# Kernel tuning notes

Measured on AMD Instinct MI355X. Metric: run time of the kernel, lower is better.

## Reference

```python
import jax, jax.numpy as jnp
import numpy as np

T = 32
BATCH = 1024
LATENT = 1024
HIDDEN = 1024


def setup_inputs() -> dict:
    key = jax.random.key(0)
    ks = jax.random.split(key, 13)
    s = 0.02
    return {
        "latent": jax.random.normal(ks[0], (BATCH, LATENT), jnp.float32),
        "h0": jax.random.normal(ks[1], (BATCH, HIDDEN), jnp.float32),
        "c0": jax.random.normal(ks[2], (BATCH, HIDDEN), jnp.float32),
        # LSTM kernel (input dim = 2*LATENT), recurrent kernel, bias; gate order i,f,g,o
        "Wk": jax.random.normal(ks[3], (2 * LATENT, 4 * HIDDEN), jnp.float32) * s,
        "Wr": jax.random.normal(ks[4], (HIDDEN, 4 * HIDDEN), jnp.float32) * s,
        "b": jnp.zeros((4 * HIDDEN,), jnp.float32),
        # attention: w1 on latent, w2 on concat(h,c)
        "W1": jax.random.normal(ks[5], (LATENT, LATENT), jnp.float32) * s,
        "b1": jnp.zeros((LATENT,), jnp.float32),
        "W2": jax.random.normal(ks[6], (2 * HIDDEN, LATENT), jnp.float32) * s,
        "b2": jnp.zeros((LATENT,), jnp.float32),
        # output mu dense
        "Wmu": jax.random.normal(ks[7], (HIDDEN, 1), jnp.float32) * s,
        "bmu": jnp.zeros((1,), jnp.float32),
    }


def _attention_context(h, c, latent, W1, b1, W2, b2):
    # score: (batch, latent_dims); softmax over feature axis (axis=1) as in the original
    query = jnp.concatenate([h, c], axis=-1)
    score = jnp.tanh(latent @ W1 + b1 + query @ W2 + b2)
    beta = jax.nn.softmax(score, axis=1)
    return beta * latent


def reference(latent, h0, c0, Wk, Wr, b, W1, b1, W2, b2, Wmu, bmu):
    # initial attention/context from h0, c0
    context = _attention_context(h0, c0, latent, W1, b1, W2, b2)

    def step(carry, _):
        h, c, ctx = carry
        x = jnp.concatenate([latent, ctx], axis=-1)  # (batch, 2*latent)
        z = x @ Wk + h @ Wr + b                       # (batch, 4*hidden)
        i, f, g, o = jnp.split(z, 4, axis=-1)         # keras gate order i,f,c,o
        c_new = jax.nn.sigmoid(f) * c + jax.nn.sigmoid(i) * jnp.tanh(g)
        h_new = jax.nn.sigmoid(o) * jnp.tanh(c_new)
        ctx_new = _attention_context(h_new, c_new, latent, W1, b1, W2, b2)
        out = h_new @ Wmu + bmu                        # (batch, 1)
        return (h_new, c_new, ctx_new), out

    _, outs = jax.lax.scan(step, (h0, c0, context), None, length=T)
    # outs: (T, batch, 1) -> (batch, T, 1)
    return jnp.transpose(outs, (1, 0, 2))
```

## Files before the change

kernel.cpp:

```cpp
#include <hip/hip_runtime.h>


#define T_ 32

typedef __attribute__((ext_vector_type(8))) short short8;
typedef __attribute__((ext_vector_type(4))) float f32x4;

__device__ __forceinline__ unsigned short bf16u(float x) {
  unsigned int u = __float_as_uint(x);
  u += 0x7FFFu + ((u >> 16) & 1u);
  return (unsigned short)(u >> 16);
}
__device__ __forceinline__ float b2f(unsigned short u) {
  return __uint_as_float(((unsigned int)u) << 16);
}
__device__ __forceinline__ ushort4 pack4(float a, float b, float c, float d) {
  ushort4 v; v.x = bf16u(a); v.y = bf16u(b); v.z = bf16u(c); v.w = bf16u(d); return v;
}
__device__ __forceinline__ float sigmoidf_(float x) { return 1.f / (1.f + __expf(-x)); }
__device__ __forceinline__ float tanhf_(float x) { return 1.f - 2.f / (__expf(2.f * x) + 1.f); }

__global__ void k_transpose(const float* __restrict__ src, int srcN,
                            unsigned short* __restrict__ dst, int dstStride, int dstColOff) {
  __shared__ float tile[32][33];
  int n0 = blockIdx.x * 32, k0 = blockIdx.y * 32;
  int tx = threadIdx.x, ty = threadIdx.y;
#pragma unroll
  for (int i = 0; i < 4; ++i)
    tile[ty + i * 8][tx] = src[(size_t)(k0 + ty + i * 8) * srcN + n0 + tx];
  __syncthreads();
#pragma unroll
  for (int i = 0; i < 4; ++i)
    dst[(size_t)(n0 + ty + i * 8) * dstStride + dstColOff + k0 + tx] = bf16u(tile[tx][ty + i * 8]);
}

__global__ __launch_bounds__(256) void k_init(const float* __restrict__ h0,
                                              const float* __restrict__ c0,
                                              const float* __restrict__ latent,
                                              unsigned short* __restrict__ A1,
                                              unsigned short* __restrict__ A2,
                                              unsigned short* __restrict__ latbf,
                                              float* __restrict__ c_st) {
  int r = blockIdx.x; int j = threadIdx.x * 4;
  const float4 hv = *(const float4*)&h0[(size_t)r * 1024 + j];
  const float4 cv = *(const float4*)&c0[(size_t)r * 1024 + j];
  const float4 lv = *(const float4*)&latent[(size_t)r * 1024 + j];
  *(ushort4*)&A2[(size_t)r * 2048 + j]        = pack4(hv.x, hv.y, hv.z, hv.w);
  *(ushort4*)&A2[(size_t)r * 2048 + 1024 + j] = pack4(cv.x, cv.y, cv.z, cv.w);
  *(ushort4*)&A1[(size_t)r * 2048 + 1024 + j] = pack4(hv.x, hv.y, hv.z, hv.w);
  *(ushort4*)&latbf[(size_t)r * 1024 + j]     = pack4(lv.x, lv.y, lv.z, lv.w);
  *(float4*)&c_st[(size_t)r * 1024 + j] = cv;
}

__global__ void k_bias(const float* __restrict__ b1, const float* __restrict__ b2,
                       float* __restrict__ bias_s) {
  int i = blockIdx.x * 256 + threadIdx.x;
  bias_s[i] = b1[i] + b2[i];
}

__global__ __launch_bounds__(256) void k_gemm(const unsigned short* __restrict__ A, int lda,
                                              const unsigned short* __restrict__ Bt, int ldb,
                                              int Kchunk,
                                              const float* __restrict__ bias,
                                              float* __restrict__ Cf,
                                              unsigned short* __restrict__ Cb, int N) {
  __shared__ unsigned short Al[2][128 * 64];
  __shared__ unsigned short Bl[2][128 * 64];
  const int tid = threadIdx.x;
  const int w = tid >> 6, l = tid & 63;
  const int row0 = blockIdx.y * 128, col0 = blockIdx.x * 128;
  const int wr = (w >> 1) * 64, wc = (w & 1) * 64;
  const int lr = l & 15, lkb = (l >> 4) * 8;
  const int srow = (l >> 3);
  const int scol_src = ((l & 7) ^ srow) * 8;
  const int kbeg = blockIdx.z * Kchunk;
  const int nsteps = Kchunk >> 6;

  f32x4 acc[4][4] = {};

  auto stage = [&](int buf, int k0) {
#pragma unroll
    for (int it = 0; it < 4; ++it) {
      int chunk = w * 4 + it;
      int r = chunk * 8 + srow;
      const unsigned short* ga = A + (size_t)(row0 + r) * lda + k0 + scol_src;
      const unsigned short* gb = Bt + (size_t)(col0 + r) * ldb + k0 + scol_src;
      __builtin_amdgcn_global_load_lds(
          (const __attribute__((address_space(1))) unsigned int*)ga,
          (__attribute__((address_space(3))) unsigned int*)((char*)&Al[buf][0] + chunk * 1024), 16, 0, 0);
      __builtin_amdgcn_global_load_lds(
          (const __attribute__((address_space(1))) unsigned int*)gb,
          (__attribute__((address_space(3))) unsigned int*)((char*)&Bl[buf][0] + chunk * 1024), 16, 0, 0);
    }
  };

  stage(0, kbeg);
  __syncthreads();
  int cur = 0;
  for (int s = 0; s < nsteps; ++s) {
    if (s + 1 < nsteps) stage(cur ^ 1, kbeg + (s + 1) * 64);
#pragma unroll
    for (int kk = 0; kk < 2; ++kk) {
      const int c2 = kk * 64 + (l >> 4) * 16;
      short8 a[4], b[4];
#pragma unroll
      for (int m = 0; m < 4; ++m) {
        int r = wr + m * 16 + lr;
        a[m] = *(const short8*)((char*)&Al[cur][0] + r * 128 + (c2 ^ ((r & 7) << 4)));
      }
#pragma unroll
      for (int n = 0; n < 4; ++n) {
        int r = wc + n * 16 + lr;
        b[n] = *(const short8*)((char*)&Bl[cur][0] + r * 128 + (c2 ^ ((r & 7) << 4)));
      }
#pragma unroll
      for (int m = 0; m < 4; ++m)
#pragma unroll
        for (int n = 0; n < 4; ++n)
          acc[m][n] = __builtin_amdgcn_mfma_f32_16x16x32_bf16(a[m], b[n], acc[m][n], 0, 0, 0);
    }
    __syncthreads();
    cur ^= 1;
  }

  const int rbase = (l >> 4) * 4;
  if (Cf) {
#pragma unroll
    for (int m = 0; m < 4; ++m)
#pragma unroll
      for (int rg = 0; rg < 4; ++rg) {
        int row = row0 + wr + m * 16 + rbase + rg;
#pragma unroll
        for (int n = 0; n < 4; ++n) {
          int col = col0 + wc + n * 16 + lr;
          Cf[(size_t)row * N + col] = acc[m][n][rg] + bias[col];
        }
      }
  } else {
    unsigned short* Cp = Cb + (size_t)blockIdx.z * (size_t)(gridDim.y * 128) * N;
#pragma unroll
    for (int m = 0; m < 4; ++m)
#pragma unroll
      for (int rg = 0; rg < 4; ++rg) {
        int row = row0 + wr + m * 16 + rbase + rg;
#pragma unroll
        for (int n = 0; n < 4; ++n) {
          int col = col0 + wc + n * 16 + lr;
          Cp[(size_t)row * N + col] = bf16u(acc[m][n][rg]);
        }
      }
  }
}

__global__ __launch_bounds__(256) void k_lstm(const float* __restrict__ z_lat,
                                              const unsigned short* __restrict__ zp,
                                              float* __restrict__ c_st,
                                              unsigned short* __restrict__ A1,
                                              unsigned short* __restrict__ A2,
                                              const float* __restrict__ Wmu,
                                              const float* __restrict__ bmu,
                                              float* __restrict__ out, int t) {
  __shared__ float red[4];
  const size_t Z1 = (size_t)1024 * 4096;
  int r = blockIdx.x; int tid = threadIdx.x; int j = tid * 4;
  float g4[4][4];
#pragma unroll
  for (int g = 0; g < 4; ++g) {
    const float4 zl = *(const float4*)&z_lat[(size_t)r * 4096 + g * 1024 + j];
    const ushort4 p0 = *(const ushort4*)&zp[(size_t)r * 4096 + g * 1024 + j];
    const ushort4 p1 = *(const ushort4*)&zp[Z1 + (size_t)r * 4096 + g * 1024 + j];
    g4[g][0] = zl.x + b2f(p0.x) + b2f(p1.x);
    g4[g][1] = zl.y + b2f(p0.y) + b2f(p1.y);
    g4[g][2] = zl.z + b2f(p0.z) + b2f(p1.z);
    g4[g][3] = zl.w + b2f(p0.w) + b2f(p1.w);
  }
  const float4 cv = *(const float4*)&c_st[(size_t)r * 1024 + j];
  const float4 wm = *(const float4*)&Wmu[j];
  float cc[4] = {cv.x, cv.y, cv.z, cv.w}, wv[4] = {wm.x, wm.y, wm.z, wm.w};
  float cn[4], hn[4];
  float part = 0.f;
#pragma unroll
  for (int q = 0; q < 4; ++q) {
    float c2 = sigmoidf_(g4[1][q]) * cc[q] + sigmoidf_(g4[0][q]) * tanhf_(g4[2][q]);
    float h2 = sigmoidf_(g4[3][q]) * tanhf_(c2);
    cn[q] = c2; hn[q] = h2; part += h2 * wv[q];
  }
  *(float4*)&c_st[(size_t)r * 1024 + j] = make_float4(cn[0], cn[1], cn[2], cn[3]);
  *(ushort4*)&A2[(size_t)r * 2048 + j]        = pack4(hn[0], hn[1], hn[2], hn[3]);
  *(ushort4*)&A2[(size_t)r * 2048 + 1024 + j] = pack4(cn[0], cn[1], cn[2], cn[3]);
  *(ushort4*)&A1[(size_t)r * 2048 + 1024 + j] = pack4(hn[0], hn[1], hn[2], hn[3]);
#pragma unroll
  for (int off = 32; off > 0; off >>= 1) part += __shfl_down(part, off, 64);
  if ((tid & 63) == 0) red[tid >> 6] = part;
  __syncthreads();
  if (tid == 0) out[(size_t)r * T_ + t] = red[0] + red[1] + red[2] + red[3] + bmu[0];
}

__global__ __launch_bounds__(256) void k_attn(const float* __restrict__ s_lat,
                                              const unsigned short* __restrict__ sp8,
                                              const float* __restrict__ latent,
                                              unsigned short* __restrict__ A1) {
  __shared__ float red[4];
  const size_t P = (size_t)1024 * 1024;
  int r = blockIdx.x; int tid = threadIdx.x; int j = tid * 4;
  const float4 sl = *(const float4*)&s_lat[(size_t)r * 1024 + j];
  float sv[4] = {sl.x, sl.y, sl.z, sl.w};
#pragma unroll
  for (int sidx = 0; sidx < 8; ++sidx) {
    const ushort4 q = *(const ushort4*)&sp8[sidx * P + (size_t)r * 1024 + j];
    sv[0] += b2f(q.x); sv[1] += b2f(q.y); sv[2] += b2f(q.z); sv[3] += b2f(q.w);
  }
  float s[4] = {tanhf_(sv[0]), tanhf_(sv[1]), tanhf_(sv[2]), tanhf_(sv[3])};
  float mx = fmaxf(fmaxf(s[0], s[1]), fmaxf(s[2], s[3]));
#pragma unroll
  for (int off = 32; off > 0; off >>= 1) mx = fmaxf(mx, __shfl_xor(mx, off, 64));
  if ((tid & 63) == 0) red[tid >> 6] = mx;
  __syncthreads();
  mx = fmaxf(fmaxf(red[0], red[1]), fmaxf(red[2], red[3]));
  __syncthreads();
  float e[4], ps = 0.f;
#pragma unroll
  for (int q = 0; q < 4; ++q) { e[q] = __expf(s[q] - mx); ps += e[q]; }
#pragma unroll
  for (int off = 32; off > 0; off >>= 1) ps += __shfl_xor(ps, off, 64);
  if ((tid & 63) == 0) red[tid >> 6] = ps;
  __syncthreads();
  float inv = 1.f / (red[0] + red[1] + red[2] + red[3]);
  const float4 lv = *(const float4*)&latent[(size_t)r * 1024 + j];
  float lvv[4] = {lv.x, lv.y, lv.z, lv.w};
  *(ushort4*)&A1[(size_t)r * 2048 + j] =
      pack4(e[0] * inv * lvv[0], e[1] * inv * lvv[1], e[2] * inv * lvv[2], e[3] * inv * lvv[3]);
}

extern "C" void kernel_launch(void* const* d_in, const int* in_sizes, int n_in,
                              void* d_out, int out_size, void* d_ws, size_t ws_size,
                              hipStream_t stream) {
  const float* latent = (const float*)d_in[0];
  const float* h0  = (const float*)d_in[1];
  const float* c0  = (const float*)d_in[2];
  const float* Wk  = (const float*)d_in[3];
  const float* Wr  = (const float*)d_in[4];
  const float* b   = (const float*)d_in[5];
  const float* W1  = (const float*)d_in[6];
  const float* b1  = (const float*)d_in[7];
  const float* W2  = (const float*)d_in[8];
  const float* b2  = (const float*)d_in[9];
  const float* Wmu = (const float*)d_in[10];
  const float* bmu = (const float*)d_in[11];
  float* out = (float*)d_out;

  char* p = (char*)d_ws;
  auto alloc = [&](size_t bytes) { void* r = (void*)p; p += (bytes + 255) & ~(size_t)255; return r; };
  unsigned short* Wzh_t = (unsigned short*)alloc((size_t)4096 * 2048 * 2);
  unsigned short* Wk1_t = (unsigned short*)alloc((size_t)4096 * 1024 * 2);
  unsigned short* W1t   = (unsigned short*)alloc((size_t)1024 * 1024 * 2);
  unsigned short* W2t   = (unsigned short*)alloc((size_t)1024 * 2048 * 2);
  unsigned short* latbf = (unsigned short*)alloc((size_t)1024 * 1024 * 2);
  unsigned short* A1    = (unsigned short*)alloc((size_t)1024 * 2048 * 2);
  unsigned short* A2    = (unsigned short*)alloc((size_t)1024 * 2048 * 2);
  float* z_lat  = (float*)alloc((size_t)1024 * 4096 * 4);
  float* s_lat  = (float*)alloc((size_t)1024 * 1024 * 4);
  unsigned short* z_part = (unsigned short*)alloc((size_t)2 * 1024 * 4096 * 2);
  unsigned short* spre_p = (unsigned short*)alloc((size_t)8 * 1024 * 1024 * 2);
  float* c_st   = (float*)alloc((size_t)1024 * 1024 * 4);
  float* bias_s = (float*)alloc((size_t)1024 * 4);

  dim3 tb(32, 8);
  k_transpose<<<dim3(128, 32), tb, 0, stream>>>(Wk, 4096, Wk1_t, 1024, 0);
  k_transpose<<<dim3(128, 32), tb, 0, stream>>>(Wk + (size_t)1024 * 4096, 4096, Wzh_t, 2048, 0);
  k_transpose<<<dim3(128, 32), tb, 0, stream>>>(Wr, 4096, Wzh_t, 2048, 1024);
  k_transpose<<<dim3(32, 64), tb, 0, stream>>>(W2, 1024, W2t, 2048, 0);
  k_transpose<<<dim3(32, 32), tb, 0, stream>>>(W1, 1024, W1t, 1024, 0);

  k_init<<<1024, 256, 0, stream>>>(h0, c0, latent, A1, A2, latbf, c_st);
  k_bias<<<4, 256, 0, stream>>>(b1, b2, bias_s);

  k_gemm<<<dim3(32, 8, 1), 256, 0, stream>>>(latbf, 1024, Wk1_t, 1024, 1024, b, z_lat, nullptr, 4096);
  k_gemm<<<dim3(8, 8, 1), 256, 0, stream>>>(latbf, 1024, W1t, 1024, 1024, bias_s, s_lat, nullptr, 1024);

  k_gemm<<<dim3(8, 8, 8), 256, 0, stream>>>(A2, 2048, W2t, 2048, 256, nullptr, nullptr, spre_p, 1024);
  k_attn<<<1024, 256, 0, stream>>>(s_lat, spre_p, latent, A1);

  for (int t = 0; t < T_; ++t) {
    k_gemm<<<dim3(32, 8, 2), 256, 0, stream>>>(A1, 2048, Wzh_t, 2048, 1024, nullptr, nullptr, z_part, 4096);
    k_lstm<<<1024, 256, 0, stream>>>(z_lat, z_part, c_st, A1, A2, Wmu, bmu, out, t);
    if (t < T_ - 1) {
      k_gemm<<<dim3(8, 8, 8), 256, 0, stream>>>(A2, 2048, W2t, 2048, 256, nullptr, nullptr, spre_p, 1024);
      k_attn<<<1024, 256, 0, stream>>>(s_lat, spre_p, latent, A1);
    }
  }
}
```

Before: 1.641 ms.

## Merge attention-query and recurrent GEMMs into one launch, shrink K tile

The recurrent h@Wr product is split out of the big per-step gate GEMM and computed together with the attention query GEMM (concat(h,c)@W2) in a single combined kernel launch, since both depend only on the new h,c. The gate GEMM then only multiplies ctx@Wk_bottom and accumulates onto the precomputed bf16 partials. The K tile drops from 64 to 32 with smaller LDS buffers, and split-K for the attention GEMM goes from 8 to 4. This packs more blocks into each launch and cuts the serial K length of the critical-path GEMM. The cost is an extra bf16 read-modify-write of the partial sums, with added rounding error.

```diff
diff --git a/kernel.cpp b/kernel.cpp
--- a/kernel.cpp
+++ b/kernel.cpp
@@ -5,6 +5,7 @@
 
 typedef __attribute__((ext_vector_type(8))) short short8;
 typedef __attribute__((ext_vector_type(4))) float f32x4;
+typedef unsigned short ushort_t;
 
 __device__ __forceinline__ unsigned short bf16u(float x) {
   unsigned int u = __float_as_uint(x);
@@ -21,7 +22,7 @@
 __device__ __forceinline__ float tanhf_(float x) { return 1.f - 2.f / (__expf(2.f * x) + 1.f); }
 
 __global__ void k_transpose(const float* __restrict__ src, int srcN,
-                            unsigned short* __restrict__ dst, int dstStride, int dstColOff) {
+                            unsigned short* __restrict__ dst, int dstStride) {
   __shared__ float tile[32][33];
   int n0 = blockIdx.x * 32, k0 = blockIdx.y * 32;
   int tx = threadIdx.x, ty = threadIdx.y;
@@ -31,13 +32,12 @@
   __syncthreads();
 #pragma unroll
   for (int i = 0; i < 4; ++i)
-    dst[(size_t)(n0 + ty + i * 8) * dstStride + dstColOff + k0 + tx] = bf16u(tile[tx][ty + i * 8]);
+    dst[(size_t)(n0 + ty + i * 8) * dstStride + k0 + tx] = bf16u(tile[tx][ty + i * 8]);
 }
 
 __global__ __launch_bounds__(256) void k_init(const float* __restrict__ h0,
                                               const float* __restrict__ c0,
                                               const float* __restrict__ latent,
-                                              unsigned short* __restrict__ A1,
                                               unsigned short* __restrict__ A2,
                                               unsigned short* __restrict__ latbf,
                                               float* __restrict__ c_st) {
@@ -47,7 +47,6 @@
   const float4 lv = *(const float4*)&latent[(size_t)r * 1024 + j];
   *(ushort4*)&A2[(size_t)r * 2048 + j]        = pack4(hv.x, hv.y, hv.z, hv.w);
   *(ushort4*)&A2[(size_t)r * 2048 + 1024 + j] = pack4(cv.x, cv.y, cv.z, cv.w);
-  *(ushort4*)&A1[(size_t)r * 2048 + 1024 + j] = pack4(hv.x, hv.y, hv.z, hv.w);
   *(ushort4*)&latbf[(size_t)r * 1024 + j]     = pack4(lv.x, lv.y, lv.z, lv.w);
   *(float4*)&c_st[(size_t)r * 1024 + j] = cv;
 }
@@ -56,6 +55,60 @@
                        float* __restrict__ bias_s) {
   int i = blockIdx.x * 256 + threadIdx.x;
   bias_s[i] = b1[i] + b2[i];
+}
+
+#define GLD(src, dst)                                                                   \
+  __builtin_amdgcn_global_load_lds(                                                     \
+      (const __attribute__((address_space(1))) unsigned int*)(src),                     \
+      (__attribute__((address_space(3))) unsigned int*)(dst), 16, 0, 0)
+
+__device__ __forceinline__ void gemm_core(const unsigned short* __restrict__ A, int lda,
+                                          const unsigned short* __restrict__ Bt, int ldb,
+                                          int row0, int col0, int kbeg, int nsteps,
+                                          unsigned short* Al, unsigned short* Bl,
+                                          f32x4 acc[4][4], int w, int l) {
+  const int lr = l & 15;
+  const int slot = l >> 4;
+  const int st_row = l >> 2;
+  const int st_cole = (((l & 3) ^ ((l >> 2) & 3)) << 3);
+  const int wr = (w >> 1) * 64, wc = (w & 1) * 64;
+
+  auto stage = [&](int buf, int k0) {
+#pragma unroll
+    for (int it = 0; it < 2; ++it) {
+      int chunk = w * 2 + it;
+      int r = chunk * 16 + st_row;
+      const unsigned short* ga = A + (size_t)(row0 + r) * lda + k0 + st_cole;
+      const unsigned short* gb = Bt + (size_t)(col0 + r) * ldb + k0 + st_cole;
+      GLD(ga, (char*)Al + buf * 8192 + chunk * 1024);
+      GLD(gb, (char*)Bl + buf * 8192 + chunk * 1024);
+    }
+  };
+
+  stage(0, kbeg);
+  __syncthreads();
+  int cur = 0;
+  for (int s = 0; s < nsteps; ++s) {
+    if (s + 1 < nsteps) stage(cur ^ 1, kbeg + (s + 1) * 32);
+    short8 a[4], b[4];
+#pragma unroll
+    for (int m = 0; m < 4; ++m) {
+      int r = wr + m * 16 + lr;
+      a[m] = *(const short8*)((char*)Al + cur * 8192 + r * 64 + ((slot ^ (r & 3)) << 4));
+    }
+#pragma unroll
+    for (int n = 0; n < 4; ++n) {
+      int r = wc + n * 16 + lr;
+      b[n] = *(const short8*)((char*)Bl + cur * 8192 + r * 64 + ((slot ^ (r & 3)) << 4));
+    }
+#pragma unroll
+    for (int m = 0; m < 4; ++m)
+#pragma unroll
+      for (int n = 0; n < 4; ++n)
+        acc[m][n] = __builtin_amdgcn_mfma_f32_16x16x32_bf16(a[m], b[n], acc[m][n], 0, 0, 0);
+    __syncthreads();
+    cur ^= 1;
+  }
 }
 
 __global__ __launch_bounds__(256) void k_gemm(const unsigned short* __restrict__ A, int lda,
@@ -63,99 +116,88 @@
                                               int Kchunk,
                                               const float* __restrict__ bias,
                                               float* __restrict__ Cf,
-                                              unsigned short* __restrict__ Cb, int N) {
-  __shared__ unsigned short Al[2][128 * 64];
-  __shared__ unsigned short Bl[2][128 * 64];
-  const int tid = threadIdx.x;
-  const int w = tid >> 6, l = tid & 63;
+                                              unsigned short* __restrict__ Cb,
+                                              const unsigned short* __restrict__ addb, int N) {
+  __shared__ unsigned short Al[2][128 * 32];
+  __shared__ unsigned short Bl[2][128 * 32];
+  const int tid = threadIdx.x, w = tid >> 6, l = tid & 63;
   const int row0 = blockIdx.y * 128, col0 = blockIdx.x * 128;
-  const int wr = (w >> 1) * 64, wc = (w & 1) * 64;
-  const int lr = l & 15, lkb = (l >> 4) * 8;
-  const int srow = (l >> 3);
-  const int scol_src = ((l & 7) ^ srow) * 8;
-  const int kbeg = blockIdx.z * Kchunk;
-  const int nsteps = Kchunk >> 6;
-
   f32x4 acc[4][4] = {};
-
-  auto stage = [&](int buf, int k0) {
-#pragma unroll
-    for (int it = 0; it < 4; ++it) {
-      int chunk = w * 4 + it;
-      int r = chunk * 8 + srow;
-      const unsigned short* ga = A + (size_t)(row0 + r) * lda + k0 + scol_src;
-      const unsigned short* gb = Bt + (size_t)(col0 + r) * ldb + k0 + scol_src;
-      __builtin_amdgcn_global_load_lds(
-          (const __attribute__((address_space(1))) unsigned int*)ga,
-          (__attribute__((address_space(3))) unsigned int*)((char*)&Al[buf][0] + chunk * 1024), 16, 0, 0);
-      __builtin_amdgcn_global_load_lds(
-          (const __attribute__((address_space(1))) unsigned int*)gb,
-          (__attribute__((address_space(3))) unsigned int*)((char*)&Bl[buf][0] + chunk * 1024), 16, 0, 0);
-    }
-  };
-
-  stage(0, kbeg);
-  __syncthreads();
-  int cur = 0;
-  for (int s = 0; s < nsteps; ++s) {
-    if (s + 1 < nsteps) stage(cur ^ 1, kbeg + (s + 1) * 64);
-#pragma unroll
-    for (int kk = 0; kk < 2; ++kk) {
-      const int c2 = kk * 64 + (l >> 4) * 16;
-      short8 a[4], b[4];
-#pragma unroll
-      for (int m = 0; m < 4; ++m) {
-        int r = wr + m * 16 + lr;
-        a[m] = *(const short8*)((char*)&Al[cur][0] + r * 128 + (c2 ^ ((r & 7) << 4)));
-      }
-#pragma unroll
-      for (int n = 0; n < 4; ++n) {
-        int r = wc + n * 16 + lr;
-        b[n] = *(const short8*)((char*)&Bl[cur][0] + r * 128 + (c2 ^ ((r & 7) << 4)));
-      }
-#pragma unroll
-      for (int m = 0; m < 4; ++m)
-#pragma unroll
-        for (int n = 0; n < 4; ++n)
-          acc[m][n] = __builtin_amdgcn_mfma_f32_16x16x32_bf16(a[m], b[n], acc[m][n], 0, 0, 0);
-    }
-    __syncthreads();
-    cur ^= 1;
-  }
-
-  const int rbase = (l >> 4) * 4;
+  gemm_core(A, lda, Bt, ldb, row0, col0, blockIdx.z * Kchunk, Kchunk >> 5,
+            &Al[0][0], &Bl[0][0], acc, w, l);
+
+  const int lr = l & 15, rbase = (l >> 4) * 4;
   if (Cf) {
 #pragma unroll
     for (int m = 0; m < 4; ++m)
 #pragma unroll
       for (int rg = 0; rg < 4; ++rg) {
-        int row = row0 + wr + m * 16 + rbase + rg;
+        int row = row0 + (w >> 1) * 64 + m * 16 + rbase + rg;
 #pragma unroll
         for (int n = 0; n < 4; ++n) {
-          int col = col0 + wc + n * 16 + lr;
+          int col = col0 + (w & 1) * 64 + n * 16 + lr;
           Cf[(size_t)row * N + col] = acc[m][n][rg] + bias[col];
         }
       }
   } else {
-    unsigned short* Cp = Cb + (size_t)blockIdx.z * (size_t)(gridDim.y * 128) * N;
+    size_t zoff = (size_t)blockIdx.z * 1024 * N;
 #pragma unroll
     for (int m = 0; m < 4; ++m)
 #pragma unroll
       for (int rg = 0; rg < 4; ++rg) {
-        int row = row0 + wr + m * 16 + rbase + rg;
+        int row = row0 + (w >> 1) * 64 + m * 16 + rbase + rg;
 #pragma unroll
         for (int n = 0; n < 4; ++n) {
-          int col = col0 + wc + n * 16 + lr;
-          Cp[(size_t)row * N + col] = bf16u(acc[m][n][rg]);
+          int col = col0 + (w & 1) * 64 + n * 16 + lr;
+          size_t idx = zoff + (size_t)row * N + col;
+          float v = acc[m][n][rg];
+          if (addb) v += b2f(addb[idx]);
+          Cb[idx] = bf16u(v);
         }
       }
   }
 }
 
+__global__ __launch_bounds__(256) void k_gemm_ab(const unsigned short* __restrict__ A2,
+                                                 const unsigned short* __restrict__ W2t,
+                                                 const unsigned short* __restrict__ Wrt,
+                                                 unsigned short* __restrict__ spre_p,
+                                                 unsigned short* __restrict__ zh_p) {
+  __shared__ unsigned short Al[2][128 * 32];
+  __shared__ unsigned short Bl[2][128 * 32];
+  const int tid = threadIdx.x, w = tid >> 6, l = tid & 63;
+  int bid = blockIdx.x;
+  const unsigned short *A, *Bt; unsigned short* outp;
+  int lda, ldb, N, row0, col0, z;
+  if (bid < 256) {
+    A = A2; lda = 2048; Bt = W2t; ldb = 2048; N = 1024; outp = spre_p;
+    col0 = (bid & 7) * 128; row0 = ((bid >> 3) & 7) * 128; z = bid >> 6;
+  } else {
+    bid -= 256;
+    A = A2; lda = 2048; Bt = Wrt; ldb = 1024; N = 4096; outp = zh_p;
+    col0 = (bid & 31) * 128; row0 = ((bid >> 5) & 7) * 128; z = bid >> 8;
+  }
+  f32x4 acc[4][4] = {};
+  gemm_core(A, lda, Bt, ldb, row0, col0, z * 512, 16, &Al[0][0], &Bl[0][0], acc, w, l);
+
+  const int lr = l & 15, rbase = (l >> 4) * 4;
+  size_t zoff = (size_t)z * 1024 * N;
+#pragma unroll
+  for (int m = 0; m < 4; ++m)
+#pragma unroll
+    for (int rg = 0; rg < 4; ++rg) {
+      int row = row0 + (w >> 1) * 64 + m * 16 + rbase + rg;
+#pragma unroll
+      for (int n = 0; n < 4; ++n) {
+        int col = col0 + (w & 1) * 64 + n * 16 + lr;
+        outp[zoff + (size_t)row * N + col] = bf16u(acc[m][n][rg]);
+      }
+    }
+}
+
 __global__ __launch_bounds__(256) void k_lstm(const float* __restrict__ z_lat,
-                                              const unsigned short* __restrict__ zp,
+                                              const unsigned short* __restrict__ zsum,
                                               float* __restrict__ c_st,
-                                              unsigned short* __restrict__ A1,
                                               unsigned short* __restrict__ A2,
                                               const float* __restrict__ Wmu,
                                               const float* __restrict__ bmu,
@@ -167,8 +209,8 @@
 #pragma unroll
   for (int g = 0; g < 4; ++g) {
     const float4 zl = *(const float4*)&z_lat[(size_t)r * 4096 + g * 1024 + j];
-    const ushort4 p0 = *(const ushort4*)&zp[(size_t)r * 4096 + g * 1024 + j];
-    const ushort4 p1 = *(const ushort4*)&zp[Z1 + (size_t)r * 4096 + g * 1024 + j];
+    const ushort4 p0 = *(const ushort4*)&zsum[(size_t)r * 4096 + g * 1024 + j];
+    const ushort4 p1 = *(const ushort4*)&zsum[Z1 + (size_t)r * 4096 + g * 1024 + j];
     g4[g][0] = zl.x + b2f(p0.x) + b2f(p1.x);
     g4[g][1] = zl.y + b2f(p0.y) + b2f(p1.y);
     g4[g][2] = zl.z + b2f(p0.z) + b2f(p1.z);
@@ -188,7 +230,6 @@
   *(float4*)&c_st[(size_t)r * 1024 + j] = make_float4(cn[0], cn[1], cn[2], cn[3]);
   *(ushort4*)&A2[(size_t)r * 2048 + j]        = pack4(hn[0], hn[1], hn[2], hn[3]);
   *(ushort4*)&A2[(size_t)r * 2048 + 1024 + j] = pack4(cn[0], cn[1], cn[2], cn[3]);
-  *(ushort4*)&A1[(size_t)r * 2048 + 1024 + j] = pack4(hn[0], hn[1], hn[2], hn[3]);
 #pragma unroll
   for (int off = 32; off > 0; off >>= 1) part += __shfl_down(part, off, 64);
   if ((tid & 63) == 0) red[tid >> 6] = part;
@@ -197,17 +238,17 @@
 }
 
 __global__ __launch_bounds__(256) void k_attn(const float* __restrict__ s_lat,
-                                              const unsigned short* __restrict__ sp8,
+                                              const unsigned short* __restrict__ sp4,
                                               const float* __restrict__ latent,
-                                              unsigned short* __restrict__ A1) {
+                                              unsigned short* __restrict__ ctxb) {
   __shared__ float red[4];
   const size_t P = (size_t)1024 * 1024;
   int r = blockIdx.x; int tid = threadIdx.x; int j = tid * 4;
   const float4 sl = *(const float4*)&s_lat[(size_t)r * 1024 + j];
   float sv[4] = {sl.x, sl.y, sl.z, sl.w};
 #pragma unroll
-  for (int sidx = 0; sidx < 8; ++sidx) {
-    const ushort4 q = *(const ushort4*)&sp8[sidx * P + (size_t)r * 1024 + j];
+  for (int sidx = 0; sidx < 4; ++sidx) {
+    const ushort4 q = *(const ushort4*)&sp4[sidx * P + (size_t)r * 1024 + j];
     sv[0] += b2f(q.x); sv[1] += b2f(q.y); sv[2] += b2f(q.z); sv[3] += b2f(q.w);
   }
   float s[4] = {tanhf_(sv[0]), tanhf_(sv[1]), tanhf_(sv[2]), tanhf_(sv[3])};
@@ -227,9 +268,8 @@
   __syncthreads();
   float inv = 1.f / (red[0] + red[1] + red[2] + red[3]);
   const float4 lv = *(const float4*)&latent[(size_t)r * 1024 + j];
-  float lvv[4] = {lv.x, lv.y, lv.z, lv.w};
-  *(ushort4*)&A1[(size_t)r * 2048 + j] =
-      pack4(e[0] * inv * lvv[0], e[1] * inv * lvv[1], e[2] * inv * lvv[2], e[3] * inv * lvv[3]);
+  *(ushort4*)&ctxb[(size_t)r * 1024 + j] =
+      pack4(e[0] * inv * lv.x, e[1] * inv * lv.y, e[2] * inv * lv.z, e[3] * inv * lv.w);
 }
 
 extern "C" void kernel_launch(void* const* d_in, const int* in_sizes, int n_in,
@@ -251,42 +291,40 @@
 
   char* p = (char*)d_ws;
   auto alloc = [&](size_t bytes) { void* r = (void*)p; p += (bytes + 255) & ~(size_t)255; return r; };
-  unsigned short* Wzh_t = (unsigned short*)alloc((size_t)4096 * 2048 * 2);
   unsigned short* Wk1_t = (unsigned short*)alloc((size_t)4096 * 1024 * 2);
+  unsigned short* Wkb_t = (unsigned short*)alloc((size_t)4096 * 1024 * 2);
+  unsigned short* Wrt   = (unsigned short*)alloc((size_t)4096 * 1024 * 2);
   unsigned short* W1t   = (unsigned short*)alloc((size_t)1024 * 1024 * 2);
   unsigned short* W2t   = (unsigned short*)alloc((size_t)1024 * 2048 * 2);
   unsigned short* latbf = (unsigned short*)alloc((size_t)1024 * 1024 * 2);
-  unsigned short* A1    = (unsigned short*)alloc((size_t)1024 * 2048 * 2);
   unsigned short* A2    = (unsigned short*)alloc((size_t)1024 * 2048 * 2);
+  unsigned short* ctxb  = (unsigned short*)alloc((size_t)1024 * 1024 * 2);
   float* z_lat  = (float*)alloc((size_t)1024 * 4096 * 4);
   float* s_lat  = (float*)alloc((size_t)1024 * 1024 * 4);
-  unsigned short* z_part = (unsigned short*)alloc((size_t)2 * 1024 * 4096 * 2);
-  unsigned short* spre_p = (unsigned short*)alloc((size_t)8 * 1024 * 1024 * 2);
+  unsigned short* zh_p   = (unsigned short*)alloc((size_t)2 * 1024 * 4096 * 2);
+  unsigned short* spre_p = (unsigned short*)alloc((size_t)4 * 1024 * 1024 * 2);
   float* c_st   = (float*)alloc((size_t)1024 * 1024 * 4);
   float* bias_s = (float*)alloc((size_t)1024 * 4);
 
   dim3 tb(32, 8);
-  k_transpose<<<dim3(128, 32), tb, 0, stream>>>(Wk, 4096, Wk1_t, 1024, 0);
-  k_transpose<<<dim3(128, 32), tb, 0, stream>>>(Wk + (size_t)1024 * 4096, 4096, Wzh_t, 2048, 0);
-  k_transpose<<<dim3(128, 32), tb, 0, stream>>>(Wr, 4096, Wzh_t, 2048, 1024);
-  k_transpose<<<dim3(32, 64), tb, 0, stream>>>(W2, 1024, W2t, 2048, 0);
-  k_transpose<<<dim3(32, 32), tb, 0, stream>>>(W1, 1024, W1t, 1024, 0);
-
-  k_init<<<1024, 256, 0, stream>>>(h0, c0, latent, A1, A2, latbf, c_st);
+  k_transpose<<<dim3(128, 32), tb, 0, stream>>>(Wk, 4096, Wk1_t, 1024);
+  k_transpose<<<dim3(128, 32), tb, 0, stream>>>(Wk + (size_t)1024 * 4096, 4096, Wkb_t, 1024);
+  k_transpose<<<dim3(128, 32), tb, 0, stream>>>(Wr, 4096, Wrt, 1024);
+  k_transpose<<<dim3(32, 64), tb, 0, stream>>>(W2, 1024, W2t, 2048);
+  k_transpose<<<dim3(32, 32), tb, 0, stream>>>(W1, 1024, W1t, 1024);
+
+  k_init<<<1024, 256, 0, stream>>>(h0, c0, latent, A2, latbf, c_st);
   k_bias<<<4, 256, 0, stream>>>(b1, b2, bias_s);
 
-  k_gemm<<<dim3(32, 8, 1), 256, 0, stream>>>(latbf, 1024, Wk1_t, 1024, 1024, b, z_lat, nullptr, 4096);
-  k_gemm<<<dim3(8, 8, 1), 256, 0, stream>>>(latbf, 1024, W1t, 1024, 1024, bias_s, s_lat, nullptr, 1024);
-
-  k_gemm<<<dim3(8, 8, 8), 256, 0, stream>>>(A2, 2048, W2t, 2048, 256, nullptr, nullptr, spre_p, 1024);
-  k_attn<<<1024, 256, 0, stream>>>(s_lat, spre_p, latent, A1);
+  k_gemm<<<dim3(32, 8, 1), 256, 0, stream>>>(latbf, 1024, Wk1_t, 1024, 1024, b, z_lat, nullptr, nullptr, 4096);
+  k_gemm<<<dim3(8, 8, 1), 256, 0, stream>>>(latbf, 1024, W1t, 1024, 1024, bias_s, s_lat, nullptr, nullptr, 1024);
+
+  k_gemm_ab<<<768, 256, 0, stream>>>(A2, W2t, Wrt, spre_p, zh_p);
 
   for (int t = 0; t < T_; ++t) {
-    k_gemm<<<dim3(32, 8, 2), 256, 0, stream>>>(A1, 2048, Wzh_t, 2048, 1024, nullptr, nullptr, z_part, 4096);
-    k_lstm<<<1024, 256, 0, stream>>>(z_lat, z_part, c_st, A1, A2, Wmu, bmu, out, t);
-    if (t < T_ - 1) {
-      k_gemm<<<dim3(8, 8, 8), 256, 0, stream>>>(A2, 2048, W2t, 2048, 256, nullptr, nullptr, spre_p, 1024);
-      k_attn<<<1024, 256, 0, stream>>>(s_lat, spre_p, latent, A1);
-    }
-  }
-}
+    k_attn<<<1024, 256, 0, stream>>>(s_lat, spre_p, latent, ctxb);
+    k_gemm<<<dim3(32, 8, 2), 256, 0, stream>>>(ctxb, 1024, Wkb_t, 1024, 512, nullptr, nullptr, zh_p, zh_p, 4096);
+    k_lstm<<<1024, 256, 0, stream>>>(z_lat, zh_p, c_st, A2, Wmu, bmu, out, t);
+    if (t < T_ - 1) k_gemm_ab<<<768, 256, 0, stream>>>(A2, W2t, Wrt, spre_p, zh_p);
+  }
+}
```

Result: slower. 2.065 ms (+25.9%).
